# Performance work log

Measured on AMD Instinct MI355X. Metric: run time of the kernel, lower is better.

## Reference

```python
import jax, jax.numpy as jnp
import numpy as np

N_STATE = 64   # n == m (required by the broadcast in the original forward)
SEQ_LEN = 200000


def setup_inputs() -> dict:
    key = jax.random.key(0)
    k_y, k_a, k_h = jax.random.split(key, 3)
    n = N_STATE
    # A scaled so spectral radius ~0.9 (stable recurrence), H ~ O(1) rows
    A = 0.9 * jax.random.normal(k_a, (n, n), dtype=jnp.float32) / jnp.sqrt(jnp.float32(n))
    H = jax.random.normal(k_h, (n, n), dtype=jnp.float32) / jnp.sqrt(jnp.float32(n))
    y = jax.random.normal(k_y, (n, SEQ_LEN), dtype=jnp.float32)
    L = jnp.float32(0.2)  # scalar learned gain (self.weights)
    return {"y": y, "A": A, "H": H, "L": L, "N": SEQ_LEN}


def reference(y, A, H, L, N):
    # x_{k+1} = A x_k + L * (y_k - H x_k);  yhat_k = H x_k  (pre-update state)
    # Vectorized over time with lax.scan (true sequential dependence).
    def step(x, yk):
        out = H @ x                      # [n] observation prediction at step k
        x_next = A @ x + L * (yk - out)  # [n] state update
        return x_next, out

    x0 = jnp.zeros((A.shape[0],), dtype=y.dtype)
    _, yhat_t = jax.lax.scan(step, x0, y.T)  # scan over time axis: y.T is [N, m]
    return yhat_t.T                          # [m, N]
```

## Files before the change

### kernel.cpp

```cpp
#include <hip/hip_runtime.h>


#define CHUNK 64
#define LOOKBACK 8

__device__ __forceinline__ float bcast(float x, int l) {
  return __uint_as_float(__builtin_amdgcn_readlane(__float_as_uint(x), l));
}

__global__ __launch_bounds__(1024) void kf_setup(const float* __restrict__ A,
                                                 const float* __restrict__ Hm,
                                                 const float* __restrict__ Lp,
                                                 float* __restrict__ ws) {
  __shared__ __align__(16) float s0[64 * 68];
  __shared__ __align__(16) float s1[64 * 68];
  const float Lg = Lp[0];
  const int t  = threadIdx.x;
  const int r  = t >> 4;
  const int c0 = (t & 15) * 4;

  if (t < 512) ws[7 * 4096 + t] = 0.f;

  {
    const float4 a4 = *(const float4*)(A  + r * 64 + c0);
    const float4 h4 = *(const float4*)(Hm + r * 64 + c0);
    float4 m4;
    m4.x = fmaf(-Lg, h4.x, a4.x);
    m4.y = fmaf(-Lg, h4.y, a4.y);
    m4.z = fmaf(-Lg, h4.z, a4.z);
    m4.w = fmaf(-Lg, h4.w, a4.w);
    *(float4*)(s0 + r * 68 + c0) = m4;
  }
  __syncthreads();

  float* src = s0;
  float* dst = s1;
  for (int sq = 0; sq < 6; ++sq) {
    *(float4*)(ws + sq * 4096 + r * 64 + c0) = *(const float4*)(src + r * 68 + c0);
    float4 acc = make_float4(0.f, 0.f, 0.f, 0.f);
    const float* srow = src + r * 68;
    #pragma unroll 8
    for (int k = 0; k < 64; ++k) {
      const float  a  = srow[k];
      const float4 b4 = *(const float4*)(src + k * 68 + c0);
      acc.x = fmaf(a, b4.x, acc.x);
      acc.y = fmaf(a, b4.y, acc.y);
      acc.z = fmaf(a, b4.z, acc.z);
      acc.w = fmaf(a, b4.w, acc.w);
    }
    __syncthreads();
    *(float4*)(dst + r * 68 + c0) = acc;
    __syncthreads();
    float* tmp = src; src = dst; dst = tmp;
  }
  *(float4*)(ws + 6 * 4096 + r * 64 + c0) = *(const float4*)(src + r * 68 + c0);
}

__global__ __launch_bounds__(64, 2) void kf_scan(const float* __restrict__ y,
                                                 const float* __restrict__ A,
                                                 const float* __restrict__ Hm,
                                                 const float* __restrict__ Lp,
                                                 float* __restrict__ bb,
                                                 float* __restrict__ X,
                                                 int Nv, int P) {
  const int lane = threadIdx.x;
  const float Lg = Lp[0];
  const int c0 = min(2 * (int)blockIdx.x,     P - 1);
  const int c1 = min(2 * (int)blockIdx.x + 1, P - 1);

  float Mrow[64];
  {
    const float* Ar = A  + lane * 64;
    const float* Hr = Hm + lane * 64;
    #pragma unroll
    for (int j = 0; j < 64; j += 4) {
      const float4 a4 = *(const float4*)(Ar + j);
      const float4 h4 = *(const float4*)(Hr + j);
      Mrow[j + 0] = fmaf(-Lg, h4.x, a4.x);
      Mrow[j + 1] = fmaf(-Lg, h4.y, a4.y);
      Mrow[j + 2] = fmaf(-Lg, h4.z, a4.z);
      Mrow[j + 3] = fmaf(-Lg, h4.w, a4.w);
    }
  }

  const float* yr0 = y + (size_t)lane * (size_t)Nv + c0 * CHUNK;
  const float* yr1 = y + (size_t)lane * (size_t)Nv + c1 * CHUNK;
  float*       X0  = X + (size_t)lane * (size_t)Nv + c0 * CHUNK;
  float*       X1  = X + (size_t)lane * (size_t)Nv + c1 * CHUNK;
  float x0 = 0.f, x1 = 0.f;

  #pragma unroll 1
  for (int t = 0; t < 8; ++t) {
    const float4 pa0 = *(const float4*)(yr0 + 8 * t);
    const float4 pb0 = *(const float4*)(yr0 + 8 * t + 4);
    const float4 pa1 = *(const float4*)(yr1 + 8 * t);
    const float4 pb1 = *(const float4*)(yr1 + 8 * t + 4);
    const float yb0[8] = {pa0.x, pa0.y, pa0.z, pa0.w, pb0.x, pb0.y, pb0.z, pb0.w};
    const float yb1[8] = {pa1.x, pa1.y, pa1.z, pa1.w, pb1.x, pb1.y, pb1.z, pb1.w};
    float xb0[8], xb1[8];

    #pragma unroll
    for (int kk = 0; kk < 8; ++kk) {
      xb0[kk] = x0;
      xb1[kk] = x1;
      float a0 = 0.f, a1 = 0.f, b0 = 0.f, b1 = 0.f;
      #pragma unroll
      for (int j = 0; j < 64; j += 2) {
        const float s0 = bcast(x0, j);
        const float s1 = bcast(x1, j);
        const float u0 = bcast(x0, j + 1);
        const float u1 = bcast(x1, j + 1);
        a0 = fmaf(Mrow[j],     s0, a0);
        b0 = fmaf(Mrow[j],     s1, b0);
        a1 = fmaf(Mrow[j + 1], u0, a1);
        b1 = fmaf(Mrow[j + 1], u1, b1);
      }
      x0 = fmaf(Lg, yb0[kk], a0 + a1);
      x1 = fmaf(Lg, yb1[kk], b0 + b1);
    }
    *(float4*)(X0 + 8 * t)     = make_float4(xb0[0], xb0[1], xb0[2], xb0[3]);
    *(float4*)(X0 + 8 * t + 4) = make_float4(xb0[4], xb0[5], xb0[6], xb0[7]);
    *(float4*)(X1 + 8 * t)     = make_float4(xb1[0], xb1[1], xb1[2], xb1[3]);
    *(float4*)(X1 + 8 * t + 4) = make_float4(xb1[4], xb1[5], xb1[6], xb1[7]);
  }
  bb[c0 * 64 + lane] = x0;
  bb[c1 * 64 + lane] = x1;
}

__global__ __launch_bounds__(64, 2) void kf_zh(const float* __restrict__ Hm,
                                               const float* __restrict__ ws,
                                               const float* __restrict__ bb,
                                               float* xo, int Nv) {
  const int lane = threadIdx.x;
  const int c    = (int)blockIdx.x;
  __shared__ __align__(16) float z[64][68];

  float s;
  {
    float Prow[64];
    #pragma unroll
    for (int j = 0; j < 64; j += 4) {
      const float4 p4 = *(const float4*)(ws + 6 * 4096 + lane * 64 + j);
      Prow[j + 0] = p4.x; Prow[j + 1] = p4.y;
      Prow[j + 2] = p4.z; Prow[j + 3] = p4.w;
    }
    s = bb[(c - LOOKBACK) * 64 + lane];
    #pragma unroll 1
    for (int t = LOOKBACK - 1; t >= 1; --t) {
      float a0 = 0.f, a1 = 0.f;
      #pragma unroll
      for (int j = 0; j < 64; j += 2) {
        a0 = fmaf(Prow[j],     bcast(s, j),     a0);
        a1 = fmaf(Prow[j + 1], bcast(s, j + 1), a1);
      }
      s = (a0 + a1) + bb[(c - t) * 64 + lane];
    }
  }

  z[lane][0] = s;
  __syncthreads();

  #pragma unroll 1
  for (int t = 0; t < 6; ++t) {
    float Mp[64];
    #pragma unroll
    for (int j = 0; j < 64; j += 4) {
      const float4 m4 = *(const float4*)(ws + t * 4096 + lane * 64 + j);
      Mp[j + 0] = m4.x; Mp[j + 1] = m4.y;
      Mp[j + 2] = m4.z; Mp[j + 3] = m4.w;
    }
    const int w = 1 << t;
    if (w < 4) {
      #pragma unroll
      for (int k = 0; k < 2; ++k) {
        if (k < w) {
          float a0 = 0.f, a1 = 0.f;
          #pragma unroll
          for (int j = 0; j < 64; j += 2) {
            a0 = fmaf(Mp[j],     z[j][k],     a0);
            a1 = fmaf(Mp[j + 1], z[j + 1][k], a1);
          }
          z[lane][k + w] = a0 + a1;
        }
      }
    } else {
      #pragma unroll 1
      for (int k = 0; k < w; k += 4) {
        float a0 = 0.f, a1 = 0.f, a2 = 0.f, a3 = 0.f;
        #pragma unroll
        for (int j = 0; j < 64; ++j) {
          const float4 zv = *(const float4*)&z[j][k];
          const float  m  = Mp[j];
          a0 = fmaf(m, zv.x, a0);
          a1 = fmaf(m, zv.y, a1);
          a2 = fmaf(m, zv.z, a2);
          a3 = fmaf(m, zv.w, a3);
        }
        *(float4*)&z[lane][k + w] = make_float4(a0, a1, a2, a3);
      }
    }
    __syncthreads();
  }

  float zcol[64];
  {
    const float* xc = xo + (size_t)c * CHUNK + lane;
    #pragma unroll 8
    for (int j = 0; j < 64; ++j) {
      zcol[j] = z[j][lane] + xc[(size_t)j * (size_t)Nv];
    }
  }

  float* oc = xo + (size_t)c * CHUNK + lane;
  #pragma unroll 1
  for (int r = 0; r < 64; ++r) {
    const float* hr = Hm + r * 64;
    float a0 = 0.f, a1 = 0.f;
    #pragma unroll
    for (int j = 0; j < 64; j += 2) {
      a0 = fmaf(hr[j],     zcol[j],     a0);
      a1 = fmaf(hr[j + 1], zcol[j + 1], a1);
    }
    oc[(size_t)r * (size_t)Nv] = a0 + a1;
  }
}

extern "C" void kernel_launch(void* const* d_in, const int* in_sizes, int n_in,
                              void* d_out, int out_size, void* d_ws, size_t ws_size,
                              hipStream_t stream) {
  const float* y  = (const float*)d_in[0];
  const float* A  = (const float*)d_in[1];
  const float* Hm = (const float*)d_in[2];
  const float* Lp = (const float*)d_in[3];
  const int Nv = in_sizes[0] / 64;
  const int P  = (Nv + CHUNK - 1) / CHUNK;

  float* ws = (float*)d_ws;
  float* bb = ws + 7 * 4096 + 512;

  kf_setup<<<1, 1024, 0, stream>>>(A, Hm, Lp, ws);
  kf_scan<<<(P + 1) / 2, 64, 0, stream>>>(y, A, Hm, Lp, bb, (float*)d_out, Nv, P);
  kf_zh<<<P, 64, 0, stream>>>(Hm, ws, bb, (float*)d_out, Nv);
}
```

Before: 279.6 us.

## Split scan chunks across waves and stage H in LDS for output projection

The scan kernel now gives each wavefront one chunk inside 256-thread blocks instead of interleaving two chunks per single-wave block, so the serial matvec chain per wave is half as long but four waves share a block. The zh kernel packs two chunks per block with per-wave LDS tiles. It computes the first powers of M directly with register broadcasts, which removes the per-step block barriers. It also stages H in LDS for the output projection instead of reading it from global memory. The aim is more parallel waves and fewer barriers and global loads, at the cost of losing the ILP from two interleaved chains and using more LDS per block.

```diff
diff --git a/kernel.cpp b/kernel.cpp
--- a/kernel.cpp
+++ b/kernel.cpp
@@ -6,6 +6,16 @@
 
 __device__ __forceinline__ float bcast(float x, int l) {
   return __uint_as_float(__builtin_amdgcn_readlane(__float_as_uint(x), l));
+}
+
+__device__ __forceinline__ float rlmv(const float* row, float v) {
+  float a0 = 0.f, a1 = 0.f;
+  #pragma unroll
+  for (int j = 0; j < 64; j += 2) {
+    a0 = fmaf(row[j],     bcast(v, j),     a0);
+    a1 = fmaf(row[j + 1], bcast(v, j + 1), a1);
+  }
+  return a0 + a1;
 }
 
 __global__ __launch_bounds__(1024) void kf_setup(const float* __restrict__ A,
@@ -56,17 +66,17 @@
   *(float4*)(ws + 6 * 4096 + r * 64 + c0) = *(const float4*)(src + r * 68 + c0);
 }
 
-__global__ __launch_bounds__(64, 2) void kf_scan(const float* __restrict__ y,
-                                                 const float* __restrict__ A,
-                                                 const float* __restrict__ Hm,
-                                                 const float* __restrict__ Lp,
-                                                 float* __restrict__ bb,
-                                                 float* __restrict__ X,
-                                                 int Nv, int P) {
-  const int lane = threadIdx.x;
+__global__ __launch_bounds__(256, 2) void kf_scan(const float* __restrict__ y,
+                                                  const float* __restrict__ A,
+                                                  const float* __restrict__ Hm,
+                                                  const float* __restrict__ Lp,
+                                                  float* __restrict__ bb,
+                                                  float* __restrict__ X,
+                                                  int Nv, int P) {
+  const int lane = threadIdx.x & 63;
+  const int wv   = threadIdx.x >> 6;
+  const int c    = min(4 * (int)blockIdx.x + wv, P - 1);
   const float Lg = Lp[0];
-  const int c0 = min(2 * (int)blockIdx.x,     P - 1);
-  const int c1 = min(2 * (int)blockIdx.x + 1, P - 1);
 
   float Mrow[64];
   {
@@ -83,57 +93,42 @@
     }
   }
 
-  const float* yr0 = y + (size_t)lane * (size_t)Nv + c0 * CHUNK;
-  const float* yr1 = y + (size_t)lane * (size_t)Nv + c1 * CHUNK;
-  float*       X0  = X + (size_t)lane * (size_t)Nv + c0 * CHUNK;
-  float*       X1  = X + (size_t)lane * (size_t)Nv + c1 * CHUNK;
-  float x0 = 0.f, x1 = 0.f;
+  const float* yr = y + (size_t)lane * (size_t)Nv + c * CHUNK;
+  float*       Xr = X + (size_t)lane * (size_t)Nv + c * CHUNK;
+  float x = 0.f;
 
   #pragma unroll 1
   for (int t = 0; t < 8; ++t) {
-    const float4 pa0 = *(const float4*)(yr0 + 8 * t);
-    const float4 pb0 = *(const float4*)(yr0 + 8 * t + 4);
-    const float4 pa1 = *(const float4*)(yr1 + 8 * t);
-    const float4 pb1 = *(const float4*)(yr1 + 8 * t + 4);
-    const float yb0[8] = {pa0.x, pa0.y, pa0.z, pa0.w, pb0.x, pb0.y, pb0.z, pb0.w};
-    const float yb1[8] = {pa1.x, pa1.y, pa1.z, pa1.w, pb1.x, pb1.y, pb1.z, pb1.w};
-    float xb0[8], xb1[8];
-
+    const float4 p0 = *(const float4*)(yr + 8 * t);
+    const float4 p1 = *(const float4*)(yr + 8 * t + 4);
+    const float yb[8] = {p0.x, p0.y, p0.z, p0.w, p1.x, p1.y, p1.z, p1.w};
+    float xb[8];
     #pragma unroll
     for (int kk = 0; kk < 8; ++kk) {
-      xb0[kk] = x0;
-      xb1[kk] = x1;
-      float a0 = 0.f, a1 = 0.f, b0 = 0.f, b1 = 0.f;
+      xb[kk] = x;
+      float a0 = 0.f, a1 = 0.f;
       #pragma unroll
       for (int j = 0; j < 64; j += 2) {
-        const float s0 = bcast(x0, j);
-        const float s1 = bcast(x1, j);
-        const float u0 = bcast(x0, j + 1);
-        const float u1 = bcast(x1, j + 1);
-        a0 = fmaf(Mrow[j],     s0, a0);
-        b0 = fmaf(Mrow[j],     s1, b0);
-        a1 = fmaf(Mrow[j + 1], u0, a1);
-        b1 = fmaf(Mrow[j + 1], u1, b1);
+        a0 = fmaf(Mrow[j],     bcast(x, j),     a0);
+        a1 = fmaf(Mrow[j + 1], bcast(x, j + 1), a1);
       }
-      x0 = fmaf(Lg, yb0[kk], a0 + a1);
-      x1 = fmaf(Lg, yb1[kk], b0 + b1);
-    }
-    *(float4*)(X0 + 8 * t)     = make_float4(xb0[0], xb0[1], xb0[2], xb0[3]);
-    *(float4*)(X0 + 8 * t + 4) = make_float4(xb0[4], xb0[5], xb0[6], xb0[7]);
-    *(float4*)(X1 + 8 * t)     = make_float4(xb1[0], xb1[1], xb1[2], xb1[3]);
-    *(float4*)(X1 + 8 * t + 4) = make_float4(xb1[4], xb1[5], xb1[6], xb1[7]);
-  }
-  bb[c0 * 64 + lane] = x0;
-  bb[c1 * 64 + lane] = x1;
-}
-
-__global__ __launch_bounds__(64, 2) void kf_zh(const float* __restrict__ Hm,
-                                               const float* __restrict__ ws,
-                                               const float* __restrict__ bb,
-                                               float* xo, int Nv) {
-  const int lane = threadIdx.x;
-  const int c    = (int)blockIdx.x;
-  __shared__ __align__(16) float z[64][68];
+      x = fmaf(Lg, yb[kk], a0 + a1);
+    }
+    *(float4*)(Xr + 8 * t)     = make_float4(xb[0], xb[1], xb[2], xb[3]);
+    *(float4*)(Xr + 8 * t + 4) = make_float4(xb[4], xb[5], xb[6], xb[7]);
+  }
+  bb[c * 64 + lane] = x;
+}
+
+__global__ __launch_bounds__(128, 2) void kf_zh(const float* __restrict__ Hm,
+                                                const float* __restrict__ ws,
+                                                const float* __restrict__ bb,
+                                                float* xo, int Nv, int P) {
+  const int lane = threadIdx.x & 63;
+  const int wv   = threadIdx.x >> 6;
+  const int c    = min(2 * (int)blockIdx.x + wv, P - 1);
+  __shared__ __align__(16) float z[2][64][68];
+  float (*zw)[68] = z[wv];
 
   float s;
   {
@@ -147,21 +142,26 @@
     s = bb[(c - LOOKBACK) * 64 + lane];
     #pragma unroll 1
     for (int t = LOOKBACK - 1; t >= 1; --t) {
-      float a0 = 0.f, a1 = 0.f;
-      #pragma unroll
-      for (int j = 0; j < 64; j += 2) {
-        a0 = fmaf(Prow[j],     bcast(s, j),     a0);
-        a1 = fmaf(Prow[j + 1], bcast(s, j + 1), a1);
-      }
-      s = (a0 + a1) + bb[(c - t) * 64 + lane];
-    }
-  }
-
-  z[lane][0] = s;
-  __syncthreads();
+      s = rlmv(Prow, s) + bb[(c - t) * 64 + lane];
+    }
+  }
+
+  {
+    float Mr[64];
+    #pragma unroll
+    for (int j = 0; j < 64; j += 4) {
+      const float4 m4 = *(const float4*)(ws + lane * 64 + j);
+      Mr[j + 0] = m4.x; Mr[j + 1] = m4.y;
+      Mr[j + 2] = m4.z; Mr[j + 3] = m4.w;
+    }
+    const float z1 = rlmv(Mr, s);
+    const float z2 = rlmv(Mr, z1);
+    const float z3 = rlmv(Mr, z2);
+    *(float4*)&zw[lane][0] = make_float4(s, z1, z2, z3);
+  }
 
   #pragma unroll 1
-  for (int t = 0; t < 6; ++t) {
+  for (int t = 2; t < 6; ++t) {
     float Mp[64];
     #pragma unroll
     for (int j = 0; j < 64; j += 4) {
@@ -170,36 +170,20 @@
       Mp[j + 2] = m4.z; Mp[j + 3] = m4.w;
     }
     const int w = 1 << t;
-    if (w < 4) {
+    #pragma unroll 1
+    for (int k = 0; k < w; k += 4) {
+      float a0 = 0.f, a1 = 0.f, a2 = 0.f, a3 = 0.f;
       #pragma unroll
-      for (int k = 0; k < 2; ++k) {
-        if (k < w) {
-          float a0 = 0.f, a1 = 0.f;
-          #pragma unroll
-          for (int j = 0; j < 64; j += 2) {
-            a0 = fmaf(Mp[j],     z[j][k],     a0);
-            a1 = fmaf(Mp[j + 1], z[j + 1][k], a1);
-          }
-          z[lane][k + w] = a0 + a1;
-        }
+      for (int j = 0; j < 64; ++j) {
+        const float4 zv = *(const float4*)&zw[j][k];
+        const float  m  = Mp[j];
+        a0 = fmaf(m, zv.x, a0);
+        a1 = fmaf(m, zv.y, a1);
+        a2 = fmaf(m, zv.z, a2);
+        a3 = fmaf(m, zv.w, a3);
       }
-    } else {
-      #pragma unroll 1
-      for (int k = 0; k < w; k += 4) {
-        float a0 = 0.f, a1 = 0.f, a2 = 0.f, a3 = 0.f;
-        #pragma unroll
-        for (int j = 0; j < 64; ++j) {
-          const float4 zv = *(const float4*)&z[j][k];
-          const float  m  = Mp[j];
-          a0 = fmaf(m, zv.x, a0);
-          a1 = fmaf(m, zv.y, a1);
-          a2 = fmaf(m, zv.z, a2);
-          a3 = fmaf(m, zv.w, a3);
-        }
-        *(float4*)&z[lane][k + w] = make_float4(a0, a1, a2, a3);
-      }
-    }
-    __syncthreads();
+      *(float4*)&zw[lane][k + w] = make_float4(a0, a1, a2, a3);
+    }
   }
 
   float zcol[64];
@@ -207,19 +191,32 @@
     const float* xc = xo + (size_t)c * CHUNK + lane;
     #pragma unroll 8
     for (int j = 0; j < 64; ++j) {
-      zcol[j] = z[j][lane] + xc[(size_t)j * (size_t)Nv];
-    }
-  }
+      zcol[j] = zw[j][lane] + xc[(size_t)j * (size_t)Nv];
+    }
+  }
+  __syncthreads();
+
+  float* Hs = &z[0][0][0];
+  #pragma unroll
+  for (int idx = threadIdx.x; idx < 1024; idx += 128) {
+    const int r  = idx >> 4;
+    const int sg = (idx & 15) * 4;
+    *(float4*)&Hs[r * 68 + sg] = *(const float4*)(Hm + r * 64 + sg);
+  }
+  __syncthreads();
 
   float* oc = xo + (size_t)c * CHUNK + lane;
-  #pragma unroll 1
+  #pragma unroll 2
   for (int r = 0; r < 64; ++r) {
-    const float* hr = Hm + r * 64;
+    const float* hr = &Hs[r * 68];
     float a0 = 0.f, a1 = 0.f;
     #pragma unroll
-    for (int j = 0; j < 64; j += 2) {
-      a0 = fmaf(hr[j],     zcol[j],     a0);
-      a1 = fmaf(hr[j + 1], zcol[j + 1], a1);
+    for (int j = 0; j < 64; j += 4) {
+      const float4 h4 = *(const float4*)(hr + j);
+      a0 = fmaf(h4.x, zcol[j + 0], a0);
+      a1 = fmaf(h4.y, zcol[j + 1], a1);
+      a0 = fmaf(h4.z, zcol[j + 2], a0);
+      a1 = fmaf(h4.w, zcol[j + 3], a1);
     }
     oc[(size_t)r * (size_t)Nv] = a0 + a1;
   }
@@ -239,6 +236,6 @@
   float* bb = ws + 7 * 4096 + 512;
 
   kf_setup<<<1, 1024, 0, stream>>>(A, Hm, Lp, ws);
-  kf_scan<<<(P + 1) / 2, 64, 0, stream>>>(y, A, Hm, Lp, bb, (float*)d_out, Nv, P);
-  kf_zh<<<P, 64, 0, stream>>>(Hm, ws, bb, (float*)d_out, Nv);
-}
+  kf_scan<<<(P + 3) / 4, 256, 0, stream>>>(y, A, Hm, Lp, bb, (float*)d_out, Nv, P);
+  kf_zh<<<(P + 1) / 2, 128, 0, stream>>>(Hm, ws, bb, (float*)d_out, Nv, P);
+}
```

After: 294.2 us. +5.2%, slower.
